# Kernel tuning notes

Hardware: AMD Instinct MI355X
Metric: run time of the kernel (lower is better)

Reference implementation:

```python
import jax, jax.numpy as jnp
import numpy as np

B = 32          # number of graphs
N_PER = 1000    # num_nodes per graph (CDSQN.num_nodes)
TOTAL = B * N_PER
E = 512000      # edges (avg degree 16)
F_IN = 128      # node_feat_dim
HID = 128       # hidden_dim (= GNN embedding_dim)
D = 64          # dsf_hidden_dim
NH = 3          # num_heads
EPS = 1e-6


def setup_inputs() -> dict:
    key = jax.random.key(0)
    ks = jax.random.split(key, 12)
    x = jax.random.normal(ks[0], (TOTAL, F_IN), jnp.float32)
    edge_index = jax.random.randint(ks[1], (2, E), 0, TOTAL, dtype=jnp.int64)
    batch_index = jnp.repeat(jnp.arange(B, dtype=jnp.int64), N_PER)
    actions = (jax.random.uniform(ks[2], (B, N_PER)) < 0.1).astype(jnp.float32)

    def lin(k, fan_in, fan_out):
        s = 1.0 / np.sqrt(fan_in)
        return jax.random.uniform(k, (fan_in, fan_out), jnp.float32, -s, s)

    Wc1 = lin(ks[3], F_IN, HID); bc1 = jnp.zeros((HID,), jnp.float32)
    Wc2 = lin(ks[4], HID, HID);  bc2 = jnp.zeros((HID,), jnp.float32)
    Wc3 = lin(ks[5], HID, HID);  bc3 = jnp.zeros((HID,), jnp.float32)
    Wg1 = lin(ks[6], HID, NH * N_PER * D); bg1 = jnp.full((NH * N_PER * D,), 0.1, jnp.float32)
    Wg2 = lin(ks[7], HID, NH * D * D);     bg2 = jnp.full((NH * D * D,), 0.1, jnp.float32)
    Wg3 = lin(ks[8], HID, NH * D);         bg3 = jnp.full((NH * D,), 0.1, jnp.float32)
    return dict(x=x, edge_index=edge_index, batch_index=batch_index, actions=actions,
                Wc1=Wc1, bc1=bc1, Wc2=Wc2, bc2=bc2, Wc3=Wc3, bc3=bc3,
                Wg1=Wg1, bg1=bg1, Wg2=Wg2, bg2=bg2, Wg3=Wg3, bg3=bg3)


def _gcn(h, W, b, src, dst, norm):
    # PyG GCNConv: h' = D^-1/2 (A+I) D^-1/2 (h W) + b ; src/dst include self loops
    h = h @ W
    msgs = h[src] * norm[:, None]            # [E+TOTAL, out]
    return jax.ops.segment_sum(msgs, dst, num_segments=TOTAL) + b


def reference(x, edge_index, batch_index, actions,
              Wc1, bc1, Wc2, bc2, Wc3, bc3,
              Wg1, bg1, Wg2, bg2, Wg3, bg3):
    loops = jnp.arange(TOTAL, dtype=edge_index.dtype)
    src = jnp.concatenate([edge_index[0], loops])
    dst = jnp.concatenate([edge_index[1], loops])
    deg = jax.ops.segment_sum(jnp.ones(src.shape[0], x.dtype), dst, num_segments=TOTAL)
    dinv = jnp.where(deg > 0, jax.lax.rsqrt(deg), 0.0)
    norm = dinv[src] * dinv[dst]

    h = jax.nn.relu(_gcn(x, Wc1, bc1, src, dst, norm))
    h = jax.nn.relu(_gcn(h, Wc2, bc2, src, dst, norm))
    h = _gcn(h, Wc3, bc3, src, dst, norm)

    # global_mean_pool
    cnt = jax.ops.segment_sum(jnp.ones(TOTAL, x.dtype), batch_index, num_segments=B)
    h_g = jax.ops.segment_sum(h, batch_index, num_segments=B) / cnt[:, None]  # [B, HID]

    # hypernetwork weights
    w1 = jax.nn.softplus((h_g @ Wg1 + bg1).reshape(B, NH, N_PER, D))
    w2 = jax.nn.softplus((h_g @ Wg2 + bg2).reshape(B, NH, D, D))
    w3 = jax.nn.softplus((h_g @ Wg3 + bg3).reshape(B, NH, D))

    # compute_q (2D actions branch)
    h1 = jnp.einsum('bn,bhnd->bhd', actions, w1)
    h1 = jnp.sqrt(jnp.clip(h1, 0.0) + EPS)           # SafeSqrt
    h2 = jnp.einsum('bhd,bhde->bhe', h1, w2)
    h2 = jnp.log1p(jnp.clip(h2, 0.0))                # SafeLog: log(1+clamp(x,0))
    out_heads = jnp.einsum('bhd,bhd->bh', h2, w3)    # [B, NH]
    return jnp.min(out_heads, axis=-1)               # [B]
```

## Files before the change

### kernel.cpp

```cpp
#include <hip/hip_runtime.h>
#include <hip/hip_bf16.h>
#include <math.h>

#define NB 32
#define N_PER 1000
#define TOTALN 32000
#define NE 512000
#define HID 128
#define Dh 64
#define NH 3
#define EPSV 1e-6f
#define PCH 25
#define W1CH 250

typedef __attribute__((ext_vector_type(8))) short bf16x8;
typedef __attribute__((ext_vector_type(4))) float f32x4;

__device__ __forceinline__ float softplusf(float x) {
    return fmaxf(x, 0.0f) + log1pf(expf(-fabsf(x)));
}
__device__ __forceinline__ unsigned short f2b(float f) {
    __hip_bfloat16 h = __float2bfloat16(f);
    return __builtin_bit_cast(unsigned short, h);
}
__device__ __forceinline__ float b2f(unsigned short u) {
    unsigned int x = ((unsigned int)u) << 16;
    return __builtin_bit_cast(float, x);
}

__global__ __launch_bounds__(256) void k_init_deg(float* deg) {
    int i = blockIdx.x * 256 + threadIdx.x;
    if (i < TOTALN) deg[i] = 1.0f;
}

__global__ __launch_bounds__(256) void k_deg(const int* __restrict__ ei, float* deg) {
    int e = blockIdx.x * 256 + threadIdx.x;
    if (e < NE) atomicAdd(&deg[ei[NE + e]], 1.0f);
}

__global__ __launch_bounds__(256) void k_prep(float* __restrict__ d, int* __restrict__ cnt) {
    int i = blockIdx.x * 256 + threadIdx.x;
    if (i < TOTALN) {
        float v = d[i];
        cnt[i] = (int)v - 1;
        d[i] = rsqrtf(v);
    }
}

__global__ __launch_bounds__(256) void k_scan_block(const int* __restrict__ cnt,
                                                    int* __restrict__ rowptr,
                                                    int* __restrict__ bsum) {
    __shared__ int sh[256];
    int t = threadIdx.x;
    int i = blockIdx.x * 256 + t;
    int v = cnt[i];
    sh[t] = v;
    __syncthreads();
    for (int off = 1; off < 256; off <<= 1) {
        int add = (t >= off) ? sh[t - off] : 0;
        __syncthreads();
        sh[t] += add;
        __syncthreads();
    }
    rowptr[i] = sh[t] - v;
    if (t == 255) bsum[blockIdx.x] = sh[255];
}

__global__ void k_scan_tot(int* __restrict__ bsum) {
    if (threadIdx.x == 0) {
        int run = 0;
        for (int i = 0; i < 125; ++i) { int t = bsum[i]; bsum[i] = run; run += t; }
    }
}

__global__ __launch_bounds__(256) void k_scan_add(int* __restrict__ rowptr,
                                                  const int* __restrict__ bsum,
                                                  int* __restrict__ cursor) {
    int i = blockIdx.x * 256 + threadIdx.x;
    int v = rowptr[i] + bsum[blockIdx.x];
    rowptr[i] = v;
    cursor[i] = v;
    if (i == 0) rowptr[TOTALN] = NE;
}

__global__ __launch_bounds__(256) void k_fill(const int* __restrict__ ei,
                                              const float* __restrict__ dinv,
                                              int* __restrict__ cursor,
                                              int* __restrict__ csr_src,
                                              float* __restrict__ csr_w) {
    int e = blockIdx.x * 256 + threadIdx.x;
    if (e < NE) {
        int s = ei[e], d = ei[NE + e];
        int pos = atomicAdd(&cursor[d], 1);
        csr_src[pos] = s;
        csr_w[pos] = dinv[s] * dinv[d];
    }
}

__global__ __launch_bounds__(256) void k_wcvt(const float* __restrict__ W,
                                              unsigned short* __restrict__ Wt) {
    int i = blockIdx.x * 256 + threadIdx.x;
    int k = i >> 7, c = i & 127;
    Wt[c * 128 + k] = f2b(W[i]);
}

template<int INF32>
__global__ __launch_bounds__(256) void k_mm(const void* __restrict__ Xv,
                                            const unsigned short* __restrict__ Wt,
                                            unsigned short* __restrict__ Y) {
    int tid = threadIdx.x;
    int wv = tid >> 6, l = tid & 63;
    int row0 = blockIdx.x * 64 + wv * 16;
    int r = l & 15, kc = l >> 4;
    bf16x8 a[4];
    if (INF32) {
        const float* X = (const float*)Xv;
#pragma unroll
        for (int ks = 0; ks < 4; ++ks) {
            const float* p = X + (long)(row0 + r) * 128 + ks * 32 + kc * 8;
            float4 f0 = *(const float4*)p;
            float4 f1 = *(const float4*)(p + 4);
            bf16x8 t;
            t[0] = (short)f2b(f0.x); t[1] = (short)f2b(f0.y);
            t[2] = (short)f2b(f0.z); t[3] = (short)f2b(f0.w);
            t[4] = (short)f2b(f1.x); t[5] = (short)f2b(f1.y);
            t[6] = (short)f2b(f1.z); t[7] = (short)f2b(f1.w);
            a[ks] = t;
        }
    } else {
        const unsigned short* X = (const unsigned short*)Xv;
#pragma unroll
        for (int ks = 0; ks < 4; ++ks)
            a[ks] = *(const bf16x8*)(X + (long)(row0 + r) * 128 + ks * 32 + kc * 8);
    }
    f32x4 acc[8];
#pragma unroll
    for (int nt = 0; nt < 8; ++nt) acc[nt] = (f32x4){0.f, 0.f, 0.f, 0.f};
#pragma unroll
    for (int ks = 0; ks < 4; ++ks) {
#pragma unroll
        for (int nt = 0; nt < 8; ++nt) {
            bf16x8 b = *(const bf16x8*)(Wt + (nt * 16 + r) * 128 + ks * 32 + kc * 8);
            acc[nt] = __builtin_amdgcn_mfma_f32_16x16x32_bf16(a[ks], b, acc[nt], 0, 0, 0);
        }
    }
#pragma unroll
    for (int nt = 0; nt < 8; ++nt)
#pragma unroll
        for (int j = 0; j < 4; ++j)
            Y[(long)(row0 + kc * 4 + j) * 128 + nt * 16 + r] = f2b(acc[nt][j]);
}

template<int MODE>
__global__ __launch_bounds__(256) void k_gather(const unsigned short* __restrict__ feat,
                                                unsigned short* __restrict__ out,
                                                const int* __restrict__ rowptr,
                                                const int* __restrict__ csr_src,
                                                const float* __restrict__ csr_w,
                                                const float* __restrict__ dinv,
                                                const float* __restrict__ bias) {
    int wid = threadIdx.x >> 6, lane = threadIdx.x & 63;
    int v = blockIdx.x * 4 + wid;
    const unsigned int* f2 = (const unsigned int*)feat;
    float dv = dinv[v];
    unsigned int sv = f2[v * 64 + lane];
    float acc0 = b2f((unsigned short)(sv & 0xffff)) * dv * dv;
    float acc1 = b2f((unsigned short)(sv >> 16)) * dv * dv;
    int e = rowptr[v], e1 = rowptr[v + 1];
    for (; e + 4 <= e1; e += 4) {
        int s0 = csr_src[e], s1 = csr_src[e + 1], s2 = csr_src[e + 2], s3 = csr_src[e + 3];
        float w0 = csr_w[e], w1 = csr_w[e + 1], w2 = csr_w[e + 2], w3 = csr_w[e + 3];
        unsigned int u0 = f2[s0 * 64 + lane];
        unsigned int u1 = f2[s1 * 64 + lane];
        unsigned int u2 = f2[s2 * 64 + lane];
        unsigned int u3 = f2[s3 * 64 + lane];
        acc0 += b2f((unsigned short)(u0 & 0xffff)) * w0 + b2f((unsigned short)(u1 & 0xffff)) * w1
              + b2f((unsigned short)(u2 & 0xffff)) * w2 + b2f((unsigned short)(u3 & 0xffff)) * w3;
        acc1 += b2f((unsigned short)(u0 >> 16)) * w0 + b2f((unsigned short)(u1 >> 16)) * w1
              + b2f((unsigned short)(u2 >> 16)) * w2 + b2f((unsigned short)(u3 >> 16)) * w3;
    }
    for (; e < e1; ++e) {
        int s = csr_src[e];
        float w = csr_w[e];
        unsigned int u = f2[s * 64 + lane];
        acc0 += b2f((unsigned short)(u & 0xffff)) * w;
        acc1 += b2f((unsigned short)(u >> 16)) * w;
    }
    if (MODE == 0) {
        int c = lane * 2;
        acc0 = fmaxf(acc0 + bias[c], 0.f);
        acc1 = fmaxf(acc1 + bias[c + 1], 0.f);
    }
    ((unsigned int*)out)[v * 64 + lane] =
        (unsigned int)f2b(acc0) | ((unsigned int)f2b(acc1) << 16);
}

__global__ __launch_bounds__(256) void k_pool1(const unsigned short* __restrict__ A,
                                               float* __restrict__ pp) {
    __shared__ float sh[256];
    int b = blockIdx.x / PCH, ch = blockIdx.x % PCH;
    int c = threadIdx.x & 127, half = threadIdx.x >> 7;
    float acc = 0.f;
    int n0 = ch * 40;
#pragma unroll 4
    for (int j = half; j < 40; j += 2)
        acc += b2f(A[(long)(b * N_PER + n0 + j) * 128 + c]);
    sh[threadIdx.x] = acc;
    __syncthreads();
    if (threadIdx.x < 128)
        pp[blockIdx.x * 128 + c] = sh[c] + sh[128 + c];
}

__global__ __launch_bounds__(256) void k_pool2(const float* __restrict__ pp,
                                               const float* __restrict__ bias,
                                               float* __restrict__ hg,
                                               float* __restrict__ hgT,
                                               unsigned short* __restrict__ hgB) {
    int i = blockIdx.x * 256 + threadIdx.x;
    if (i >= NB * 128) return;
    int b = i >> 7, c = i & 127;
    float s = 0.f;
#pragma unroll
    for (int ch = 0; ch < PCH; ++ch)
        s += pp[(b * PCH + ch) * 128 + c];
    float v = s * (1.0f / N_PER) + bias[c];
    hg[i] = v;
    hgT[c * NB + b] = v;
    hgB[i] = f2b(v);
}

__global__ __launch_bounds__(256) void k_w1(const unsigned short* __restrict__ hgB,
                                            const float* __restrict__ Wg1,
                                            const float* __restrict__ bg1,
                                            const float* __restrict__ actions,
                                            float* __restrict__ p1) {
    __shared__ unsigned short wt[64][136];
    int h = blockIdx.x / W1CH, chunk = blockIdx.x % W1CH;
    int tid = threadIdx.x;
    int wv = tid >> 6, l = tid & 63;
    int r = l & 15, kc = l >> 4;
    const long KS = (long)NH * N_PER * Dh;
    bf16x8 a[2][4];
#pragma unroll
    for (int mt = 0; mt < 2; ++mt)
#pragma unroll
        for (int ks = 0; ks < 4; ++ks)
            a[mt][ks] = *(const bf16x8*)(hgB + (mt * 16 + r) * 128 + ks * 32 + kc * 8);
    int sd = tid & 63, sk = tid >> 6;
    for (int nn = 0; nn < 4; ++nn) {
        int n = chunk * 4 + nn;
        long colbase = (long)h * (N_PER * Dh) + (long)n * Dh;
        __syncthreads();
        const float* Wb = Wg1 + colbase + sd;
#pragma unroll 8
        for (int it = 0; it < 32; ++it) {
            int k = it * 4 + sk;
            wt[sd][k] = f2b(Wb[(long)k * KS]);
        }
        __syncthreads();
        f32x4 acc0 = (f32x4){0.f, 0.f, 0.f, 0.f};
        f32x4 acc1 = (f32x4){0.f, 0.f, 0.f, 0.f};
#pragma unroll
        for (int ks = 0; ks < 4; ++ks) {
            bf16x8 bb = *(const bf16x8*)&wt[wv * 16 + r][ks * 32 + kc * 8];
            acc0 = __builtin_amdgcn_mfma_f32_16x16x32_bf16(a[0][ks], bb, acc0, 0, 0, 0);
            acc1 = __builtin_amdgcn_mfma_f32_16x16x32_bf16(a[1][ks], bb, acc1, 0, 0, 0);
        }
        float bgv = bg1[colbase + wv * 16 + r];
        float* po = p1 + ((long)h * N_PER + n) * 2048;
#pragma unroll
        for (int j = 0; j < 4; ++j) {
            int b0 = kc * 4 + j;
            int b1 = 16 + kc * 4 + j;
            po[b0 * 64 + wv * 16 + r] = softplusf(acc0[j] + bgv) * actions[b0 * N_PER + n];
            po[b1 * 64 + wv * 16 + r] = softplusf(acc1[j] + bgv) * actions[b1 * N_PER + n];
        }
    }
}

__global__ __launch_bounds__(256) void k_red1a(const float* __restrict__ p1,
                                               float* __restrict__ rp) {
    __shared__ float sh[4][64];
    int bh = blockIdx.x >> 3, seg = blockIdx.x & 7;
    int b = bh / 3, h = bh % 3;
    int part = threadIdx.x >> 6, d = threadIdx.x & 63;
    const float* base = p1 + (long)h * N_PER * 2048 + b * 64 + d;
    float s = 0.f;
    for (int n = seg * 125 + part; n < seg * 125 + 125; n += 4)
        s += base[(long)n * 2048];
    if (part) sh[part][d] = s;
    __syncthreads();
    if (part == 0)
        rp[((long)bh * 8 + seg) * 64 + d] = s + sh[1][d] + sh[2][d] + sh[3][d];
}

__global__ __launch_bounds__(256) void k_red1b(const float* __restrict__ rp,
                                               float* __restrict__ h1) {
    int o = blockIdx.x * 256 + threadIdx.x;
    if (o >= 96 * 64) return;
    int bh = o >> 6, d = o & 63;
    float s = 0.f;
#pragma unroll
    for (int seg = 0; seg < 8; ++seg)
        s += rp[((long)bh * 8 + seg) * 64 + d];
    h1[bh * 64 + d] = sqrtf(fmaxf(s, 0.f) + EPSV);
}

__global__ __launch_bounds__(256) void k_w2(const float* __restrict__ hg,
                                            const float* __restrict__ Wg2,
                                            const float* __restrict__ bg2,
                                            const float* __restrict__ h1,
                                            float* __restrict__ p2) {
    __shared__ float hgs[32][128];
    __shared__ float wt[128][64];
    __shared__ float h1s[32];
    int hd = blockIdx.x;
    int tid = threadIdx.x;
    for (int i = 0; i < 16; ++i) {
        int idx = tid + i * 256;
        hgs[idx >> 7][idx & 127] = hg[idx];
    }
    long base = (long)hd * 64;
    for (int i = 0; i < 32; ++i) {
        int idx = tid + i * 256;
        wt[idx >> 6][idx & 63] = Wg2[(long)(idx >> 6) * (NH * Dh * Dh) + base + (idx & 63)];
    }
    int h = hd >> 6, d = hd & 63;
    if (tid < 32) h1s[tid] = h1[tid * (NH * Dh) + h * Dh + d];
    __syncthreads();
    int e = tid & 63, bq = tid >> 6;
    float bgv = bg2[base + e];
    float dot[8];
#pragma unroll
    for (int bi = 0; bi < 8; ++bi) dot[bi] = 0.f;
    for (int k = 0; k < 128; ++k) {
        float w = wt[k][e];
#pragma unroll
        for (int bi = 0; bi < 8; ++bi)
            dot[bi] += hgs[bq * 8 + bi][k] * w;
    }
    float* po = p2 + (long)hd * (32 * 64);
#pragma unroll
    for (int bi = 0; bi < 8; ++bi) {
        int b = bq * 8 + bi;
        po[b * 64 + e] = softplusf(dot[bi] + bgv) * h1s[b];
    }
}

__global__ __launch_bounds__(256) void k_red2(const float* __restrict__ p2,
                                              float* __restrict__ h2) {
    int o = blockIdx.x * 256 + threadIdx.x;
    if (o >= 32 * 192) return;
    int bh = o >> 6;
    int h = bh % 3, b = bh / 3;
    int e = o & 63;
    float s = 0.f;
    for (int d = 0; d < 64; ++d)
        s += p2[(h * 64 + d) * 2048 + b * 64 + e];
    h2[o] = log1pf(fmaxf(s, 0.f));
}

__global__ __launch_bounds__(192) void k_out(const float* __restrict__ hg,
                                             const float* __restrict__ Wg3,
                                             const float* __restrict__ bg3,
                                             const float* __restrict__ h2,
                                             float* __restrict__ out) {
    __shared__ float hgb[128];
    __shared__ float hres[NH];
    int b = blockIdx.x, tid = threadIdx.x;
    if (tid < 128) hgb[tid] = hg[b * 128 + tid];
    __syncthreads();
    int h = tid / 64, e = tid & 63;
    int c = h * 64 + e;
    float dot = 0.f;
    for (int k = 0; k < 128; ++k)
        dot += hgb[k] * Wg3[k * (NH * Dh) + c];
    float v = softplusf(dot + bg3[c]) * h2[b * 192 + c];
    for (int off = 32; off; off >>= 1)
        v += __shfl_down(v, off, 64);
    if (e == 0) hres[h] = v;
    __syncthreads();
    if (tid == 0) out[b] = fminf(fminf(hres[0], hres[1]), hres[2]);
}

extern "C" void kernel_launch(void* const* d_in, const int* in_sizes, int n_in,
                              void* d_out, int out_size, void* d_ws, size_t ws_size,
                              hipStream_t stream) {
    const float* x   = (const float*)d_in[0];
    const int*   ei  = (const int*)d_in[1];
    const float* act = (const float*)d_in[3];
    const float* Wc1 = (const float*)d_in[4];
    const float* bc1 = (const float*)d_in[5];
    const float* Wc2 = (const float*)d_in[6];
    const float* bc2 = (const float*)d_in[7];
    const float* Wc3 = (const float*)d_in[8];
    const float* bc3 = (const float*)d_in[9];
    const float* Wg1 = (const float*)d_in[10];
    const float* bg1 = (const float*)d_in[11];
    const float* Wg2 = (const float*)d_in[12];
    const float* bg2 = (const float*)d_in[13];
    const float* Wg3 = (const float*)d_in[14];
    const float* bg3 = (const float*)d_in[15];
    float* out = (float*)d_out;

    float* ws   = (float*)d_ws;
    float* dinv = ws;
    float* bufA = dinv + TOTALN;
    float* bufB = bufA + (long)TOTALN * 128;
    float* hg   = bufB + (long)TOTALN * 128;
    float* h1   = hg + 32 * 128;
    float* h2   = h1 + 32 * 192;
    float* csr_w = h2 + 32 * 192;
    float* pp   = csr_w + NE;
    float* hgT  = pp + NB * PCH * 128;
    unsigned short* hgB = (unsigned short*)(hgT + 128 * NB);
    int* cnt    = (int*)(hgB + 4096);
    int* rowptr = cnt + TOTALN;
    int* cursor = rowptr + TOTALN + 4;
    int* bsum   = cursor + TOTALN;
    int* csr_src= bsum + 128;
    unsigned short* Wt = (unsigned short*)(csr_src + NE);
    unsigned short* fA = (unsigned short*)bufA;
    unsigned short* fB = (unsigned short*)bufB;
    float* p1   = bufA;
    float* p2   = bufA + (long)3 * N_PER * 2048;
    float* rp   = pp;

    k_init_deg<<<(TOTALN + 255) / 256, 256, 0, stream>>>(dinv);
    k_deg<<<NE / 256, 256, 0, stream>>>(ei, dinv);
    k_prep<<<(TOTALN + 255) / 256, 256, 0, stream>>>(dinv, cnt);
    k_scan_block<<<125, 256, 0, stream>>>(cnt, rowptr, bsum);
    k_scan_tot<<<1, 64, 0, stream>>>(bsum);
    k_scan_add<<<125, 256, 0, stream>>>(rowptr, bsum, cursor);
    k_fill<<<NE / 256, 256, 0, stream>>>(ei, dinv, cursor, csr_src, csr_w);

    k_wcvt<<<64, 256, 0, stream>>>(Wc1, Wt);
    k_mm<1><<<500, 256, 0, stream>>>(x, Wt, fB);
    k_gather<0><<<TOTALN / 4, 256, 0, stream>>>(fB, fA, rowptr, csr_src, csr_w, dinv, bc1);
    k_wcvt<<<64, 256, 0, stream>>>(Wc2, Wt);
    k_mm<0><<<500, 256, 0, stream>>>(fA, Wt, fB);
    k_gather<0><<<TOTALN / 4, 256, 0, stream>>>(fB, fA, rowptr, csr_src, csr_w, dinv, bc2);
    k_wcvt<<<64, 256, 0, stream>>>(Wc3, Wt);
    k_mm<0><<<500, 256, 0, stream>>>(fA, Wt, fB);
    k_gather<1><<<TOTALN / 4, 256, 0, stream>>>(fB, fA, rowptr, csr_src, csr_w, dinv, nullptr);
    k_pool1<<<NB * PCH, 256, 0, stream>>>(fA, pp);
    k_pool2<<<(NB * 128 + 255) / 256, 256, 0, stream>>>(pp, bc3, hg, hgT, hgB);

    k_w1<<<NH * W1CH, 256, 0, stream>>>(hgB, Wg1, bg1, act, p1);
    k_red1a<<<96 * 8, 256, 0, stream>>>(p1, rp);
    k_red1b<<<24, 256, 0, stream>>>(rp, h1);
    k_w2<<<NH * Dh, 256, 0, stream>>>(hg, Wg2, bg2, h1, p2);
    k_red2<<<24, 256, 0, stream>>>(p2, h2);
    k_out<<<NB, 192, 0, stream>>>(hg, Wg3, bg3, h2, out);
}
```

Baseline: 270.9 us.

## Fuse mean-pool into final gather, merge weight conversions, pre-reduce hypernet partials

The last GCN gather now reduces each block's four nodes in shared memory and atomically adds them into a per-graph pool buffer, which removes the separate pool kernel and the write of the final feature matrix. The three layer-weight conversions are merged into one launch. k_w1 now accumulates its per-node softplus·action products in registers across its four nodes and writes one partial per chunk, which cuts the p1 intermediate by 4x and collapses two reduction kernels into one. This trades some atomic contention on the 128 pool entries per graph, and floating-point summation order now varies between runs.

```diff
diff --git a/kernel.cpp b/kernel.cpp
--- a/kernel.cpp
+++ b/kernel.cpp
@@ -10,7 +10,6 @@
 #define Dh 64
 #define NH 3
 #define EPSV 1e-6f
-#define PCH 25
 #define W1CH 250
 
 typedef __attribute__((ext_vector_type(8))) short bf16x8;
@@ -28,9 +27,10 @@
     return __builtin_bit_cast(float, x);
 }
 
-__global__ __launch_bounds__(256) void k_init_deg(float* deg) {
+__global__ __launch_bounds__(256) void k_init_deg(float* deg, float* pp) {
     int i = blockIdx.x * 256 + threadIdx.x;
     if (i < TOTALN) deg[i] = 1.0f;
+    if (i < NB * 128) pp[i] = 0.f;
 }
 
 __global__ __launch_bounds__(256) void k_deg(const int* __restrict__ ei, float* deg) {
@@ -97,11 +97,15 @@
     }
 }
 
-__global__ __launch_bounds__(256) void k_wcvt(const float* __restrict__ W,
-                                              unsigned short* __restrict__ Wt) {
+__global__ __launch_bounds__(256) void k_wcvt3(const float* __restrict__ W1,
+                                               const float* __restrict__ W2,
+                                               const float* __restrict__ W3,
+                                               unsigned short* __restrict__ Wt) {
     int i = blockIdx.x * 256 + threadIdx.x;
-    int k = i >> 7, c = i & 127;
-    Wt[c * 128 + k] = f2b(W[i]);
+    int w = i >> 14, j = i & 16383;
+    const float* W = (w == 0) ? W1 : (w == 1) ? W2 : W3;
+    int k = j >> 7, c = j & 127;
+    Wt[w * 16384 + c * 128 + k] = f2b(W[j]);
 }
 
 template<int INF32>
@@ -158,7 +162,9 @@
                                                 const int* __restrict__ csr_src,
                                                 const float* __restrict__ csr_w,
                                                 const float* __restrict__ dinv,
-                                                const float* __restrict__ bias) {
+                                                const float* __restrict__ bias,
+                                                float* __restrict__ pp) {
+    __shared__ float sh[4][128];
     int wid = threadIdx.x >> 6, lane = threadIdx.x & 63;
     int v = blockIdx.x * 4 + wid;
     const unsigned int* f2 = (const unsigned int*)feat;
@@ -190,42 +196,29 @@
         int c = lane * 2;
         acc0 = fmaxf(acc0 + bias[c], 0.f);
         acc1 = fmaxf(acc1 + bias[c + 1], 0.f);
-    }
-    ((unsigned int*)out)[v * 64 + lane] =
-        (unsigned int)f2b(acc0) | ((unsigned int)f2b(acc1) << 16);
-}
-
-__global__ __launch_bounds__(256) void k_pool1(const unsigned short* __restrict__ A,
-                                               float* __restrict__ pp) {
-    __shared__ float sh[256];
-    int b = blockIdx.x / PCH, ch = blockIdx.x % PCH;
-    int c = threadIdx.x & 127, half = threadIdx.x >> 7;
-    float acc = 0.f;
-    int n0 = ch * 40;
-#pragma unroll 4
-    for (int j = half; j < 40; j += 2)
-        acc += b2f(A[(long)(b * N_PER + n0 + j) * 128 + c]);
-    sh[threadIdx.x] = acc;
-    __syncthreads();
-    if (threadIdx.x < 128)
-        pp[blockIdx.x * 128 + c] = sh[c] + sh[128 + c];
+        ((unsigned int*)out)[v * 64 + lane] =
+            (unsigned int)f2b(acc0) | ((unsigned int)f2b(acc1) << 16);
+    } else {
+        sh[wid][lane * 2] = acc0;
+        sh[wid][lane * 2 + 1] = acc1;
+        __syncthreads();
+        int tid = threadIdx.x;
+        if (tid < 128) {
+            int b = (blockIdx.x * 4) / N_PER;
+            atomicAdd(&pp[b * 128 + tid],
+                      sh[0][tid] + sh[1][tid] + sh[2][tid] + sh[3][tid]);
+        }
+    }
 }
 
 __global__ __launch_bounds__(256) void k_pool2(const float* __restrict__ pp,
                                                const float* __restrict__ bias,
                                                float* __restrict__ hg,
-                                               float* __restrict__ hgT,
                                                unsigned short* __restrict__ hgB) {
     int i = blockIdx.x * 256 + threadIdx.x;
     if (i >= NB * 128) return;
-    int b = i >> 7, c = i & 127;
-    float s = 0.f;
-#pragma unroll
-    for (int ch = 0; ch < PCH; ++ch)
-        s += pp[(b * PCH + ch) * 128 + c];
-    float v = s * (1.0f / N_PER) + bias[c];
+    float v = pp[i] * (1.0f / N_PER) + bias[i & 127];
     hg[i] = v;
-    hgT[c * NB + b] = v;
     hgB[i] = f2b(v);
 }
 
@@ -246,6 +239,8 @@
 #pragma unroll
         for (int ks = 0; ks < 4; ++ks)
             a[mt][ks] = *(const bf16x8*)(hgB + (mt * 16 + r) * 128 + ks * 32 + kc * 8);
+    float sp0[4] = {0.f, 0.f, 0.f, 0.f};
+    float sp1[4] = {0.f, 0.f, 0.f, 0.f};
     int sd = tid & 63, sk = tid >> 6;
     for (int nn = 0; nn < 4; ++nn) {
         int n = chunk * 4 + nn;
@@ -267,43 +262,35 @@
             acc1 = __builtin_amdgcn_mfma_f32_16x16x32_bf16(a[1][ks], bb, acc1, 0, 0, 0);
         }
         float bgv = bg1[colbase + wv * 16 + r];
-        float* po = p1 + ((long)h * N_PER + n) * 2048;
 #pragma unroll
         for (int j = 0; j < 4; ++j) {
             int b0 = kc * 4 + j;
             int b1 = 16 + kc * 4 + j;
-            po[b0 * 64 + wv * 16 + r] = softplusf(acc0[j] + bgv) * actions[b0 * N_PER + n];
-            po[b1 * 64 + wv * 16 + r] = softplusf(acc1[j] + bgv) * actions[b1 * N_PER + n];
-        }
-    }
-}
-
-__global__ __launch_bounds__(256) void k_red1a(const float* __restrict__ p1,
-                                               float* __restrict__ rp) {
+            sp0[j] += softplusf(acc0[j] + bgv) * actions[b0 * N_PER + n];
+            sp1[j] += softplusf(acc1[j] + bgv) * actions[b1 * N_PER + n];
+        }
+    }
+    float* po = p1 + ((long)h * W1CH + chunk) * 2048;
+#pragma unroll
+    for (int j = 0; j < 4; ++j) {
+        po[(kc * 4 + j) * 64 + wv * 16 + r] = sp0[j];
+        po[(16 + kc * 4 + j) * 64 + wv * 16 + r] = sp1[j];
+    }
+}
+
+__global__ __launch_bounds__(256) void k_red1(const float* __restrict__ p1,
+                                              float* __restrict__ h1) {
     __shared__ float sh[4][64];
-    int bh = blockIdx.x >> 3, seg = blockIdx.x & 7;
-    int b = bh / 3, h = bh % 3;
+    int b = blockIdx.x / 3, h = blockIdx.x % 3;
     int part = threadIdx.x >> 6, d = threadIdx.x & 63;
-    const float* base = p1 + (long)h * N_PER * 2048 + b * 64 + d;
+    const float* base = p1 + (long)h * W1CH * 2048 + b * 64 + d;
     float s = 0.f;
-    for (int n = seg * 125 + part; n < seg * 125 + 125; n += 4)
-        s += base[(long)n * 2048];
+    for (int ch = part; ch < W1CH; ch += 4)
+        s += base[(long)ch * 2048];
     if (part) sh[part][d] = s;
     __syncthreads();
     if (part == 0)
-        rp[((long)bh * 8 + seg) * 64 + d] = s + sh[1][d] + sh[2][d] + sh[3][d];
-}
-
-__global__ __launch_bounds__(256) void k_red1b(const float* __restrict__ rp,
-                                               float* __restrict__ h1) {
-    int o = blockIdx.x * 256 + threadIdx.x;
-    if (o >= 96 * 64) return;
-    int bh = o >> 6, d = o & 63;
-    float s = 0.f;
-#pragma unroll
-    for (int seg = 0; seg < 8; ++seg)
-        s += rp[((long)bh * 8 + seg) * 64 + d];
-    h1[bh * 64 + d] = sqrtf(fmaxf(s, 0.f) + EPSV);
+        h1[(b * 3 + h) * 64 + d] = sqrtf(fmaxf(s + sh[1][d] + sh[2][d] + sh[3][d], 0.f) + EPSV);
 }
 
 __global__ __launch_bounds__(256) void k_w2(const float* __restrict__ hg,
@@ -412,8 +399,7 @@
     float* h2   = h1 + 32 * 192;
     float* csr_w = h2 + 32 * 192;
     float* pp   = csr_w + NE;
-    float* hgT  = pp + NB * PCH * 128;
-    unsigned short* hgB = (unsigned short*)(hgT + 128 * NB);
+    unsigned short* hgB = (unsigned short*)(pp + NB * 128);
     int* cnt    = (int*)(hgB + 4096);
     int* rowptr = cnt + TOTALN;
     int* cursor = rowptr + TOTALN + 4;
@@ -423,32 +409,27 @@
     unsigned short* fA = (unsigned short*)bufA;
     unsigned short* fB = (unsigned short*)bufB;
     float* p1   = bufA;
-    float* p2   = bufA + (long)3 * N_PER * 2048;
-    float* rp   = pp;
-
-    k_init_deg<<<(TOTALN + 255) / 256, 256, 0, stream>>>(dinv);
+    float* p2   = bufA + (long)NH * W1CH * 2048;
+
+    k_init_deg<<<(TOTALN + 255) / 256, 256, 0, stream>>>(dinv, pp);
     k_deg<<<NE / 256, 256, 0, stream>>>(ei, dinv);
     k_prep<<<(TOTALN + 255) / 256, 256, 0, stream>>>(dinv, cnt);
     k_scan_block<<<125, 256, 0, stream>>>(cnt, rowptr, bsum);
     k_scan_tot<<<1, 64, 0, stream>>>(bsum);
     k_scan_add<<<125, 256, 0, stream>>>(rowptr, bsum, cursor);
     k_fill<<<NE / 256, 256, 0, stream>>>(ei, dinv, cursor, csr_src, csr_w);
-
-    k_wcvt<<<64, 256, 0, stream>>>(Wc1, Wt);
+    k_wcvt3<<<192, 256, 0, stream>>>(Wc1, Wc2, Wc3, Wt);
+
     k_mm<1><<<500, 256, 0, stream>>>(x, Wt, fB);
-    k_gather<0><<<TOTALN / 4, 256, 0, stream>>>(fB, fA, rowptr, csr_src, csr_w, dinv, bc1);
-    k_wcvt<<<64, 256, 0, stream>>>(Wc2, Wt);
-    k_mm<0><<<500, 256, 0, stream>>>(fA, Wt, fB);
-    k_gather<0><<<TOTALN / 4, 256, 0, stream>>>(fB, fA, rowptr, csr_src, csr_w, dinv, bc2);
-    k_wcvt<<<64, 256, 0, stream>>>(Wc3, Wt);
-    k_mm<0><<<500, 256, 0, stream>>>(fA, Wt, fB);
-    k_gather<1><<<TOTALN / 4, 256, 0, stream>>>(fB, fA, rowptr, csr_src, csr_w, dinv, nullptr);
-    k_pool1<<<NB * PCH, 256, 0, stream>>>(fA, pp);
-    k_pool2<<<(NB * 128 + 255) / 256, 256, 0, stream>>>(pp, bc3, hg, hgT, hgB);
+    k_gather<0><<<TOTALN / 4, 256, 0, stream>>>(fB, fA, rowptr, csr_src, csr_w, dinv, bc1, nullptr);
+    k_mm<0><<<500, 256, 0, stream>>>(fA, Wt + 16384, fB);
+    k_gather<0><<<TOTALN / 4, 256, 0, stream>>>(fB, fA, rowptr, csr_src, csr_w, dinv, bc2, nullptr);
+    k_mm<0><<<500, 256, 0, stream>>>(fA, Wt + 32768, fB);
+    k_gather<1><<<TOTALN / 4, 256, 0, stream>>>(fB, nullptr, rowptr, csr_src, csr_w, dinv, nullptr, pp);
+    k_pool2<<<(NB * 128 + 255) / 256, 256, 0, stream>>>(pp, bc3, hg, hgB);
 
     k_w1<<<NH * W1CH, 256, 0, stream>>>(hgB, Wg1, bg1, act, p1);
-    k_red1a<<<96 * 8, 256, 0, stream>>>(p1, rp);
-    k_red1b<<<24, 256, 0, stream>>>(rp, h1);
+    k_red1<<<96, 256, 0, stream>>>(p1, h1);
     k_w2<<<NH * Dh, 256, 0, stream>>>(hg, Wg2, bg2, h1, p2);
     k_red2<<<24, 256, 0, stream>>>(p2, h2);
     k_out<<<NB, 192, 0, stream>>>(hg, Wg3, bg3, h2, out);
```

After: 281.7 us. +4.0%, slower.
